# Performance work log

Measured on AMD Instinct MI355X. Metric: run time of the kernel, lower is better.

## Reference

```python
import jax, jax.numpy as jnp
import numpy as np

B, N, H, K = 8192, 256, 2048, 1
BETA = 0.99
LOG2PI = float(np.log(2.0 * np.pi))


def V(z, Wv):
    # quadratic Lyapunov-style function; one positive value per sample (keepdims)
    u = z @ Wv
    return jnp.sum(u * u, axis=-1, keepdims=True) + 1e-3


def setup_inputs() -> dict:
    key = jax.random.key(0)
    ks = jax.random.split(key, 6)
    s1 = 1.0 / np.sqrt(N)
    s2 = 1.0 / np.sqrt(H)
    return {
        "x": jax.random.normal(ks[0], (B, N), jnp.float32),
        "y": jax.random.normal(ks[1], (B, 1, N), jnp.float32),
        "eps": jax.random.normal(ks[2], (B, 1, N), jnp.float32),
        "W1": jax.random.normal(ks[3], (N, H), jnp.float32) * s1,
        "b1": jnp.zeros((H,), jnp.float32),
        "W2": jax.random.normal(ks[4], (H, 2 * N), jnp.float32) * s2,
        "b2": jnp.zeros((2 * N,), jnp.float32),
        "Wv": jax.random.normal(ks[5], (N, N), jnp.float32) * s1,
    }


def reference(x, y, eps, W1, b1, W2, b2, Wv):
    # fhat: 2-layer MLP -> [B, 2N] = concat(mu, logvar)
    h = jnp.tanh(x @ W1 + b1)
    f = h @ W2 + b2
    mu, logvar = jnp.split(f, 2, axis=-1)            # [B, K*N] each (K=1)
    # torch: stack(split(mu, N, dim=1)).view(-1, 1, N)
    mu = mu.reshape(B, K, N).transpose(1, 0, 2).reshape(B * K, 1, N)
    var = jnp.exp(logvar).reshape(B, K, N).transpose(1, 0, 2).reshape(B * K, 1, N)
    # Lyapunov rescaling of the mean (per-sample scalar scale)
    Vx = V(x, Wv)[:, None, :]                        # [B,1,1]
    Vmu = V(mu, Wv)                                  # [B,1,1]
    bVx = BETA * Vx
    mu_stable = mu * ((bVx - jax.nn.relu(bVx - Vmu)) / Vmu)
    # reparameterized sample of diagonal MVN
    fx = mu_stable + jnp.sqrt(var) * eps             # [B,1,N]
    # diagonal-MVN log_prob, single fused pass
    q = (y - mu_stable) ** 2 / var
    logp = -0.5 * (N * LOG2PI + jnp.sum(jnp.log(var) + q, axis=-1))  # [B,1]
    logp_y = -jnp.sum(logp)
    return fx, logp_y
```

## Files before the change

kernel.cpp:

```cpp
#include <hip/hip_runtime.h>
#include <stdint.h>

#define B_SZ 8192
#define N_SZ 256
#define H_SZ 2048
#define LOG2PI_F 1.8378770664093453f
#define BETA_F 0.99f

typedef unsigned short ushort_t;
typedef __attribute__((ext_vector_type(8))) __bf16 bf16x8;
typedef __attribute__((ext_vector_type(4))) float f32x4;
typedef __attribute__((ext_vector_type(8))) ushort_t u16x8;

__device__ __forceinline__ ushort_t f2bf(float f) {
    unsigned int u = __float_as_uint(f);
    unsigned int r = (u + 0x7FFFu + ((u >> 16) & 1u)) >> 16;
    return (ushort_t)r;
}

__device__ __forceinline__ float fast_tanh(float v) {
    float ex = __expf(2.0f * v);
    return 1.0f - __fdividef(2.0f, ex + 1.0f);
}

__device__ __forceinline__ void async_ld16(const void* g, const char* lds_uniform) {
    __builtin_amdgcn_global_load_lds(
        (const __attribute__((address_space(1))) void*)g,
        (__attribute__((address_space(3))) void*)lds_uniform,
        16, 0, 0);
}

__global__ __launch_bounds__(256, 4)
void gemm1_vx_kernel(const ushort_t* __restrict__ xb, const ushort_t* __restrict__ W1p,
                     const ushort_t* __restrict__ Wvp, const float* __restrict__ b1,
                     ushort_t* __restrict__ h, float* __restrict__ vx)
{
    __shared__ __align__(16) char smem[32768];
    char* sA = smem;
    char* sB = smem + 16384;
    const int tid = threadIdx.x;
    const int lane = tid & 63;
    const int w = tid >> 6;
    const int q = lane >> 4;
    const int rlo = lane & 15;
    const int wr = w >> 1, wc = w & 1;
    const int row0 = blockIdx.y * 128;

    const bool w1path = blockIdx.x < 16;
    const int n0 = (w1path ? blockIdx.x : blockIdx.x - 16) * 128;
    const ushort_t* Bp = w1path ? W1p : Wvp;
    const int N = w1path ? H_SZ : N_SZ;

    f32x4 acc[4][4];
#pragma unroll
    for (int i = 0; i < 4; ++i)
#pragma unroll
        for (int j = 0; j < 4; ++j)
            acc[i][j] = f32x4{0.f, 0.f, 0.f, 0.f};

    for (int k0 = 0; k0 < N_SZ; k0 += 64) {
        __syncthreads();
#pragma unroll
        for (int r = 0; r < 4; ++r) {
            int c = r * 256 + tid;
            int kq = c >> 7, m = c & 127;
            async_ld16(xb + (size_t)(row0 + m) * N_SZ + k0 + kq * 8, sA + (c << 4));
        }
        int ko0 = k0 >> 3;
#pragma unroll
        for (int r = 0; r < 4; ++r) {
            int c = r * 256 + tid;
            int kq = c >> 7, n = c & 127;
            async_ld16(Bp + ((size_t)(ko0 + kq) * N + n0 + n) * 8, sB + (c << 4));
        }
        __syncthreads();

#pragma unroll
        for (int ks = 0; ks < 2; ++ks) {
            int kq = ks * 4 + q;
            bf16x8 af[4], bfr[4];
#pragma unroll
            for (int i = 0; i < 4; ++i)
                af[i] = *(const bf16x8*)(sA + (((kq << 7) + wr * 64 + i * 16 + rlo) << 4));
#pragma unroll
            for (int j = 0; j < 4; ++j)
                bfr[j] = *(const bf16x8*)(sB + (((kq << 7) + wc * 64 + j * 16 + rlo) << 4));
#pragma unroll
            for (int i = 0; i < 4; ++i)
#pragma unroll
                for (int j = 0; j < 4; ++j)
                    acc[i][j] = __builtin_amdgcn_mfma_f32_16x16x32_bf16(af[i], bfr[j], acc[i][j], 0, 0, 0);
        }
    }

    if (w1path) {
#pragma unroll
        for (int j = 0; j < 4; ++j) {
            int col = n0 + wc * 64 + j * 16 + rlo;
            float bv = b1[col];
#pragma unroll
            for (int i = 0; i < 4; ++i) {
                int rowb = row0 + wr * 64 + i * 16 + q * 4;
#pragma unroll
                for (int rr = 0; rr < 4; ++rr)
                    h[(size_t)(rowb + rr) * H_SZ + col] = f2bf(fast_tanh(acc[i][j][rr] + bv));
            }
        }
    } else {
#pragma unroll
        for (int i = 0; i < 4; ++i) {
#pragma unroll
            for (int rr = 0; rr < 4; ++rr) {
                float s = 0.f;
#pragma unroll
                for (int j = 0; j < 4; ++j) { float v = acc[i][j][rr]; s += v * v; }
#pragma unroll
                for (int m = 1; m < 16; m <<= 1) s += __shfl_xor(s, m, 64);
                if (rlo == 0)
                    atomicAdd(&vx[row0 + wr * 64 + i * 16 + q * 4 + rr], s);
            }
        }
    }
}

__global__ __launch_bounds__(256, 4)
void gemm2_kernel(const ushort_t* __restrict__ h, const ushort_t* __restrict__ W2p,
                  const float* __restrict__ b2, float* __restrict__ f,
                  ushort_t* __restrict__ mub)
{
    __shared__ __align__(16) char smem[24576];
    char* sA = smem;
    char* sB = smem + 8192;
    const int tid = threadIdx.x;
    const int lane = tid & 63;
    const int w = tid >> 6;
    const int q = lane >> 4;
    const int rlo = lane & 15;
    const int wr = w >> 1, wc = w & 1;

    const int bid = blockIdx.x;
    const int r8 = bid & 7;
    const int u = bid >> 3;
    const int cb = u & 3;
    const int tb = u >> 2;
    const int row0 = (r8 + 8 * tb) * 64;
    const int n0 = cb * 128;

    f32x4 acc[2][4];
#pragma unroll
    for (int i = 0; i < 2; ++i)
#pragma unroll
        for (int j = 0; j < 4; ++j)
            acc[i][j] = f32x4{0.f, 0.f, 0.f, 0.f};

    for (int k0 = 0; k0 < H_SZ; k0 += 64) {
        __syncthreads();
#pragma unroll
        for (int r = 0; r < 2; ++r) {
            int c = r * 256 + tid;
            int kq = c >> 6, m = c & 63;
            async_ld16(h + (size_t)(row0 + m) * H_SZ + k0 + kq * 8, sA + (c << 4));
        }
        int ko0 = k0 >> 3;
#pragma unroll
        for (int r = 0; r < 4; ++r) {
            int c = r * 256 + tid;
            int kq = c >> 7, n = c & 127;
            async_ld16(W2p + ((size_t)(ko0 + kq) * 512 + n0 + n) * 8, sB + (c << 4));
        }
        __syncthreads();

#pragma unroll
        for (int ks = 0; ks < 2; ++ks) {
            int kq = ks * 4 + q;
            bf16x8 af[2], bfr[4];
#pragma unroll
            for (int i = 0; i < 2; ++i)
                af[i] = *(const bf16x8*)(sA + (((kq << 6) + wr * 32 + i * 16 + rlo) << 4));
#pragma unroll
            for (int j = 0; j < 4; ++j)
                bfr[j] = *(const bf16x8*)(sB + (((kq << 7) + wc * 64 + j * 16 + rlo) << 4));
#pragma unroll
            for (int i = 0; i < 2; ++i)
#pragma unroll
                for (int j = 0; j < 4; ++j)
                    acc[i][j] = __builtin_amdgcn_mfma_f32_16x16x32_bf16(af[i], bfr[j], acc[i][j], 0, 0, 0);
        }
    }

#pragma unroll
    for (int j = 0; j < 4; ++j) {
        int col = n0 + wc * 64 + j * 16 + rlo;
        float bv = b2[col];
#pragma unroll
        for (int i = 0; i < 2; ++i) {
            int rowb = row0 + wr * 32 + i * 16 + q * 4;
#pragma unroll
            for (int rr = 0; rr < 4; ++rr) {
                float v = acc[i][j][rr] + bv;
                f[(size_t)(rowb + rr) * 512 + col] = v;
                if (col < N_SZ)
                    mub[(size_t)(rowb + rr) * N_SZ + col] = f2bf(v);
            }
        }
    }
}

__global__ __launch_bounds__(256)
void vmu_epilogue_kernel(const ushort_t* __restrict__ mub, const ushort_t* __restrict__ Wvp,
                         const float* __restrict__ f, const float* __restrict__ y,
                         const float* __restrict__ eps, const float* __restrict__ vx,
                         float* __restrict__ out, float* __restrict__ partials)
{
    __shared__ float vsum[4][64];
    __shared__ float vmu_s[64];
    __shared__ float red[4];
    const int tid = threadIdx.x;
    const int lane = tid & 63;
    const int w = tid >> 6;
    const int q = lane >> 4;
    const int rlo = lane & 15;
    const int r0 = blockIdx.x * 64;

    f32x4 acc[4][4];
#pragma unroll
    for (int i = 0; i < 4; ++i)
#pragma unroll
        for (int j = 0; j < 4; ++j)
            acc[i][j] = f32x4{0.f, 0.f, 0.f, 0.f};

    const ushort_t* a0 = mub + (size_t)(r0 + rlo) * N_SZ + q * 8;
    const ushort_t* b0 = Wvp + ((size_t)q * N_SZ + w * 64 + rlo) * 8;
#pragma unroll
    for (int s = 0; s < 8; ++s) {
        bf16x8 af[4], bfr[4];
#pragma unroll
        for (int i = 0; i < 4; ++i)
            af[i] = *(const bf16x8*)(a0 + i * 16 * N_SZ + s * 32);
#pragma unroll
        for (int j = 0; j < 4; ++j)
            bfr[j] = *(const bf16x8*)(b0 + s * 4 * N_SZ * 8 + j * 128);
#pragma unroll
        for (int i = 0; i < 4; ++i)
#pragma unroll
            for (int j = 0; j < 4; ++j)
                acc[i][j] = __builtin_amdgcn_mfma_f32_16x16x32_bf16(af[i], bfr[j], acc[i][j], 0, 0, 0);
    }
#pragma unroll
    for (int i = 0; i < 4; ++i) {
#pragma unroll
        for (int rr = 0; rr < 4; ++rr) {
            float s = 0.f;
#pragma unroll
            for (int j = 0; j < 4; ++j) { float v = acc[i][j][rr]; s += v * v; }
#pragma unroll
            for (int m = 1; m < 16; m <<= 1) s += __shfl_xor(s, m, 64);
            if (rlo == 0) vsum[w][i * 16 + q * 4 + rr] = s;
        }
    }
    __syncthreads();
    if (tid < 64)
        vmu_s[tid] = 1e-3f + vsum[0][tid] + vsum[1][tid] + vsum[2][tid] + vsum[3][tid];
    __syncthreads();

    float t = 0.f;
    const int n = tid;
#pragma unroll 4
    for (int r = 0; r < 64; ++r) {
        size_t row = (size_t)(r0 + r);
        float mu = f[row * 512 + n];
        float lv = f[row * 512 + 256 + n];
        float var = expf(lv);
        float Vx = vx[row] + 1e-3f;
        float Vmu = vmu_s[r];
        float scale = fminf(BETA_F * Vx, Vmu) / Vmu;
        float mus = mu * scale;
        out[row * 256 + n] = mus + sqrtf(var) * eps[row * 256 + n];
        float d = y[row * 256 + n] - mus;
        t += lv + d * d / var;
    }
#pragma unroll
    for (int m = 32; m >= 1; m >>= 1) t += __shfl_down(t, m, 64);
    if (lane == 0) red[w] = t;
    __syncthreads();
    if (tid == 0)
        partials[blockIdx.x] = red[0] + red[1] + red[2] + red[3];
}

__global__ __launch_bounds__(128)
void reduce_kernel(const float* __restrict__ partials, float* __restrict__ out)
{
    int tid = threadIdx.x;
    float s = partials[tid];
#pragma unroll
    for (int m = 32; m >= 1; m >>= 1) s += __shfl_down(s, m, 64);
    __shared__ float red[2];
    if ((tid & 63) == 0) red[tid >> 6] = s;
    __syncthreads();
    if (tid == 0)
        out[(size_t)B_SZ * N_SZ] =
            0.5f * (red[0] + red[1] + (float)N_SZ * LOG2PI_F * (float)B_SZ);
}

__global__ __launch_bounds__(256)
void convert_kernel(const float* __restrict__ x, const float* __restrict__ W1,
                    const float* __restrict__ W2, const float* __restrict__ Wv,
                    ushort_t* __restrict__ xb, ushort_t* __restrict__ W1p,
                    ushort_t* __restrict__ W2p, ushort_t* __restrict__ Wvp)
{
    const int XC = 262144, W1C = 65536, W2C = 131072;
    int c = blockIdx.x * 256 + threadIdx.x;
    if (c < XC) {
        f32x4 a = *(const f32x4*)(x + (size_t)c * 8);
        f32x4 b = *(const f32x4*)(x + (size_t)c * 8 + 4);
        u16x8 o;
#pragma unroll
        for (int i = 0; i < 4; ++i) { o[i] = f2bf(a[i]); o[4 + i] = f2bf(b[i]); }
        *(u16x8*)(xb + (size_t)c * 8) = o;
    } else if (c < XC + W1C) {
        int d = c - XC;
        int ko = d >> 11, n = d & 2047;
        u16x8 o;
#pragma unroll
        for (int ki = 0; ki < 8; ++ki)
            o[ki] = f2bf(W1[(size_t)(ko * 8 + ki) * H_SZ + n]);
        *(u16x8*)(W1p + (size_t)d * 8) = o;
    } else if (c < XC + W1C + W2C) {
        int d = c - XC - W1C;
        int ko = d >> 9, n = d & 511;
        u16x8 o;
#pragma unroll
        for (int ki = 0; ki < 8; ++ki)
            o[ki] = f2bf(W2[(size_t)(ko * 8 + ki) * 512 + n]);
        *(u16x8*)(W2p + (size_t)d * 8) = o;
    } else {
        int d = c - XC - W1C - W2C;
        int ko = d >> 8, n = d & 255;
        u16x8 o;
#pragma unroll
        for (int ki = 0; ki < 8; ++ki)
            o[ki] = f2bf(Wv[(size_t)(ko * 8 + ki) * N_SZ + n]);
        *(u16x8*)(Wvp + (size_t)d * 8) = o;
    }
}

extern "C" void kernel_launch(void* const* d_in, const int* in_sizes, int n_in,
                              void* d_out, int out_size, void* d_ws, size_t ws_size,
                              hipStream_t stream)
{
    const float* x   = (const float*)d_in[0];
    const float* y   = (const float*)d_in[1];
    const float* eps = (const float*)d_in[2];
    const float* W1  = (const float*)d_in[3];
    const float* b1  = (const float*)d_in[4];
    const float* W2  = (const float*)d_in[5];
    const float* b2  = (const float*)d_in[6];
    const float* Wv  = (const float*)d_in[7];
    float* out = (float*)d_out;

    char* ws = (char*)d_ws;
    size_t off = 0;
    auto alloc = [&](size_t bytes) {
        char* p = ws + off;
        off += (bytes + 255) & ~(size_t)255;
        return p;
    };
    ushort_t* xb  = (ushort_t*)alloc((size_t)B_SZ * N_SZ * 2);
    ushort_t* W1p = (ushort_t*)alloc((size_t)N_SZ * H_SZ * 2);
    ushort_t* W2p = (ushort_t*)alloc((size_t)H_SZ * 512 * 2);
    ushort_t* Wvp = (ushort_t*)alloc((size_t)N_SZ * N_SZ * 2);
    ushort_t* h   = (ushort_t*)alloc((size_t)B_SZ * H_SZ * 2);
    float*    f   = (float*)alloc((size_t)B_SZ * 512 * 4);
    ushort_t* mub = (ushort_t*)alloc((size_t)B_SZ * N_SZ * 2);
    float*    vx  = (float*)alloc((size_t)B_SZ * 4);
    float*    partials = (float*)alloc(128 * 4);

    hipMemsetAsync(vx, 0, (size_t)B_SZ * 4, stream);

    const int TOTALC = 262144 + 65536 + 131072 + 8192;
    convert_kernel<<<TOTALC / 256, 256, 0, stream>>>(x, W1, W2, Wv, xb, W1p, W2p, Wvp);

    gemm1_vx_kernel<<<dim3(18, B_SZ / 128), 256, 0, stream>>>(xb, W1p, Wvp, b1, h, vx);
    gemm2_kernel<<<512, 256, 0, stream>>>(h, W2p, b2, f, mub);
    vmu_epilogue_kernel<<<128, 256, 0, stream>>>(mub, Wvp, f, y, eps, vx, out, partials);
    reduce_kernel<<<1, 128, 0, stream>>>(partials, out);
}
```

Measured before the change: 175.1 us.

## Split Vmu epilogue into 16-row blocks and remap GEMM1 grid for XCD locality

The Vmu/epilogue kernel now handles 16 rows per block instead of 64, so it launches 512 blocks rather than 128 and can fill all CUs on the device. The final reduction is widened to sum 512 partials. Separately, GEMM1 switches to a 1D grid with a block-index remap so that consecutive block IDs, which land on different XCDs, take different row tiles, aiming for better L2 reuse of the weight tiles. The smaller epilogue blocks re-read the Wv fragments more often in total.

After: 162.4 us. 1.08x faster.

```diff
diff --git a/kernel.cpp b/kernel.cpp
--- a/kernel.cpp
+++ b/kernel.cpp
@@ -44,10 +44,16 @@
     const int q = lane >> 4;
     const int rlo = lane & 15;
     const int wr = w >> 1, wc = w & 1;
-    const int row0 = blockIdx.y * 128;
-
-    const bool w1path = blockIdx.x < 16;
-    const int n0 = (w1path ? blockIdx.x : blockIdx.x - 16) * 128;
+
+    const int bid = blockIdx.x;
+    const int r8 = bid & 7;
+    const int u = bid >> 3;
+    const int cb = u % 18;
+    const int tb = u / 18;
+    const int row0 = (r8 + 8 * tb) * 128;
+
+    const bool w1path = cb < 16;
+    const int n0 = (w1path ? cb : cb - 16) * 128;
     const ushort_t* Bp = w1path ? W1p : Wvp;
     const int N = w1path ? H_SZ : N_SZ;
 
@@ -212,61 +218,52 @@
                          const float* __restrict__ eps, const float* __restrict__ vx,
                          float* __restrict__ out, float* __restrict__ partials)
 {
-    __shared__ float vsum[4][64];
-    __shared__ float vmu_s[64];
+    __shared__ float vsum[4][16];
+    __shared__ float vmu_s[16];
     __shared__ float red[4];
     const int tid = threadIdx.x;
     const int lane = tid & 63;
     const int w = tid >> 6;
     const int q = lane >> 4;
     const int rlo = lane & 15;
-    const int r0 = blockIdx.x * 64;
-
-    f32x4 acc[4][4];
-#pragma unroll
-    for (int i = 0; i < 4; ++i)
-#pragma unroll
-        for (int j = 0; j < 4; ++j)
-            acc[i][j] = f32x4{0.f, 0.f, 0.f, 0.f};
+    const int r0 = blockIdx.x * 16;
+
+    f32x4 acc[4];
+#pragma unroll
+    for (int j = 0; j < 4; ++j)
+        acc[j] = f32x4{0.f, 0.f, 0.f, 0.f};
 
     const ushort_t* a0 = mub + (size_t)(r0 + rlo) * N_SZ + q * 8;
     const ushort_t* b0 = Wvp + ((size_t)q * N_SZ + w * 64 + rlo) * 8;
 #pragma unroll
     for (int s = 0; s < 8; ++s) {
-        bf16x8 af[4], bfr[4];
-#pragma unroll
-        for (int i = 0; i < 4; ++i)
-            af[i] = *(const bf16x8*)(a0 + i * 16 * N_SZ + s * 32);
+        bf16x8 af = *(const bf16x8*)(a0 + s * 32);
+        bf16x8 bfr[4];
 #pragma unroll
         for (int j = 0; j < 4; ++j)
             bfr[j] = *(const bf16x8*)(b0 + s * 4 * N_SZ * 8 + j * 128);
 #pragma unroll
-        for (int i = 0; i < 4; ++i)
-#pragma unroll
-            for (int j = 0; j < 4; ++j)
-                acc[i][j] = __builtin_amdgcn_mfma_f32_16x16x32_bf16(af[i], bfr[j], acc[i][j], 0, 0, 0);
-    }
-#pragma unroll
-    for (int i = 0; i < 4; ++i) {
-#pragma unroll
-        for (int rr = 0; rr < 4; ++rr) {
-            float s = 0.f;
-#pragma unroll
-            for (int j = 0; j < 4; ++j) { float v = acc[i][j][rr]; s += v * v; }
-#pragma unroll
-            for (int m = 1; m < 16; m <<= 1) s += __shfl_xor(s, m, 64);
-            if (rlo == 0) vsum[w][i * 16 + q * 4 + rr] = s;
-        }
+        for (int j = 0; j < 4; ++j)
+            acc[j] = __builtin_amdgcn_mfma_f32_16x16x32_bf16(af, bfr[j], acc[j], 0, 0, 0);
+    }
+#pragma unroll
+    for (int rr = 0; rr < 4; ++rr) {
+        float s = 0.f;
+#pragma unroll
+        for (int j = 0; j < 4; ++j) { float v = acc[j][rr]; s += v * v; }
+#pragma unroll
+        for (int m = 1; m < 16; m <<= 1) s += __shfl_xor(s, m, 64);
+        if (rlo == 0) vsum[w][q * 4 + rr] = s;
     }
     __syncthreads();
-    if (tid < 64)
+    if (tid < 16)
         vmu_s[tid] = 1e-3f + vsum[0][tid] + vsum[1][tid] + vsum[2][tid] + vsum[3][tid];
     __syncthreads();
 
     float t = 0.f;
     const int n = tid;
 #pragma unroll 4
-    for (int r = 0; r < 64; ++r) {
+    for (int r = 0; r < 16; ++r) {
         size_t row = (size_t)(r0 + r);
         float mu = f[row * 512 + n];
         float lv = f[row * 512 + 256 + n];
@@ -287,19 +284,20 @@
         partials[blockIdx.x] = red[0] + red[1] + red[2] + red[3];
 }
 
-__global__ __launch_bounds__(128)
+__global__ __launch_bounds__(256)
 void reduce_kernel(const float* __restrict__ partials, float* __restrict__ out)
 {
     int tid = threadIdx.x;
-    float s = partials[tid];
+    float s = partials[tid] + partials[tid + 256];
 #pragma unroll
     for (int m = 32; m >= 1; m >>= 1) s += __shfl_down(s, m, 64);
-    __shared__ float red[2];
+    __shared__ float red[4];
     if ((tid & 63) == 0) red[tid >> 6] = s;
     __syncthreads();
     if (tid == 0)
         out[(size_t)B_SZ * N_SZ] =
-            0.5f * (red[0] + red[1] + (float)N_SZ * LOG2PI_F * (float)B_SZ);
+            0.5f * (red[0] + red[1] + red[2] + red[3] +
+                    (float)N_SZ * LOG2PI_F * (float)B_SZ);
 }
 
 __global__ __launch_bounds__(256)
@@ -373,15 +371,15 @@
     float*    f   = (float*)alloc((size_t)B_SZ * 512 * 4);
     ushort_t* mub = (ushort_t*)alloc((size_t)B_SZ * N_SZ * 2);
     float*    vx  = (float*)alloc((size_t)B_SZ * 4);
-    float*    partials = (float*)alloc(128 * 4);
+    float*    partials = (float*)alloc(512 * 4);
 
     hipMemsetAsync(vx, 0, (size_t)B_SZ * 4, stream);
 
     const int TOTALC = 262144 + 65536 + 131072 + 8192;
     convert_kernel<<<TOTALC / 256, 256, 0, stream>>>(x, W1, W2, Wv, xb, W1p, W2p, Wvp);
 
-    gemm1_vx_kernel<<<dim3(18, B_SZ / 128), 256, 0, stream>>>(xb, W1p, Wvp, b1, h, vx);
+    gemm1_vx_kernel<<<1152, 256, 0, stream>>>(xb, W1p, Wvp, b1, h, vx);
     gemm2_kernel<<<512, 256, 0, stream>>>(h, W2p, b2, f, mub);
-    vmu_epilogue_kernel<<<128, 256, 0, stream>>>(mub, Wvp, f, y, eps, vx, out, partials);
-    reduce_kernel<<<1, 128, 0, stream>>>(partials, out);
-}
+    vmu_epilogue_kernel<<<512, 256, 0, stream>>>(mub, Wvp, f, y, eps, vx, out, partials);
+    reduce_kernel<<<1, 256, 0, stream>>>(partials, out);
+}
```
